# Kernel tuning notes

Measured on AMD Instinct MI355X. Metric: run time of the kernel, lower is better.

The kernel has to match this reference:

```python
import jax, jax.numpy as jnp
import numpy as np

# Module hyperparameters (from init_kwargs)
LEARNING_RATE = 0.01  # not used inside compute_weight_update
TAU_PLUS = 20.0
TAU_MINUS = 20.0
A_PLUS = 0.005
A_MINUS = 0.00525
TARGET_RATE = 0.1
HOMEOSTATIC_RATE = 0.001
TAU_HOMEOSTATIC = 1000.0

B, T, N_PRE, N_POST = 16, 8192, 128, 128


def setup_inputs() -> dict:
    key = jax.random.key(0)
    k1, k2, k3 = jax.random.split(key, 3)
    # Bernoulli spike trains at ~target_rate firing probability
    pre_spikes = (jax.random.uniform(k1, (B, T, N_PRE)) < TARGET_RATE).astype(jnp.float32)
    post_spikes = (jax.random.uniform(k2, (B, T, N_POST)) < TARGET_RATE).astype(jnp.float32)
    weights = jax.random.uniform(k3, (N_PRE, N_POST), dtype=jnp.float32)
    return {"pre_spikes": pre_spikes, "post_spikes": post_spikes, "weights": weights, "dt": 1}


def _temporal_corr(x, kernel, pad):
    """Correlate x [B,T,N] along time with 1-D kernel [L], padding pad=(lo,hi)."""
    b, t, n = x.shape
    xr = jnp.moveaxis(x, 1, 2).reshape(b * n, 1, t)  # [B*N, 1, T]
    k = kernel.reshape(1, 1, -1).astype(x.dtype)
    y = jax.lax.conv_general_dilated(
        xr, k, window_strides=(1,), padding=[pad],
        dimension_numbers=("NCH", "OIH", "NCH"))
    return jnp.moveaxis(y.reshape(b, n, t), 2, 1)  # [B,T,N]


def reference(pre_spikes, post_spikes, weights, dt):
    b, t, n_pre = pre_spikes.shape
    dt = float(dt)

    # Homeostatic rate tracking (first call: avg rates initialized to target_rate)
    alpha = dt / TAU_HOMEOSTATIC
    current_post_rate = post_spikes.mean(axis=(0, 1))
    avg_post_rate = (1.0 - alpha) * TARGET_RATE + alpha * current_post_rate

    # Truncated exponential STDP window: tau in 1..min(int(3*tau)-1, ...) = 1..59
    L = int(TAU_PLUS * 3)  # 60 taps (tau=0 tap zeroed)
    taus = jnp.arange(L, dtype=jnp.float32)
    w_plus = jnp.where(taus > 0, A_PLUS * jnp.exp(-taus * dt / TAU_PLUS), 0.0)
    w_minus = jnp.where(taus > 0, A_MINUS * jnp.exp(-taus * dt / TAU_MINUS), 0.0)

    # LTP: post_filt[t] = sum_{tau>=1} w_plus[tau] * post[t+tau] (future, zero-padded)
    post_filt = _temporal_corr(post_spikes, w_plus, (0, L - 1))
    # LTD: pre_filt[t] = sum_{tau>=1} w_minus[tau] * pre[t-tau] (past, zero-padded)
    pre_filt = _temporal_corr(pre_spikes, w_minus[::-1], (L - 1, 0))

    # sum_t mean_b outer(pre[t], post_filt[t]) - outer(pre_filt[t], post[t]), then /T
    ltp = jnp.einsum("btp,btq->pq", pre_spikes, post_filt)
    ltd = jnp.einsum("btp,btq->pq", pre_filt, post_spikes)
    stdp_update = (ltp - ltd) / (b * t)

    # Homeostatic regulation pulls post rate toward target
    post_rate_error = avg_post_rate - TARGET_RATE
    homeostatic_update = -HOMEOSTATIC_RATE * post_rate_error[None, :] * weights

    return stdp_update + homeostatic_update
```

## Files before the change

### kernel.cpp

```cpp
#include <hip/hip_runtime.h>

#define BB 16
#define TT 8192
#define NN 128
constexpr int CHUNK = 256;
constexpr int NCH   = BB * TT / CHUNK;
constexpr int NBLK  = NCH / 2;
constexpr int OUTN  = NN * NN;
constexpr int GS    = 264;
constexpr int SLOTS = OUTN / 2;
constexpr int PROWS = 315;
constexpr int NWAVE = 16;
constexpr int WIN   = CHUNK / NWAVE;

typedef _Float16 f16x8 __attribute__((ext_vector_type(8)));
typedef _Float16 f16x2 __attribute__((ext_vector_type(2)));
typedef float    f32x4 __attribute__((ext_vector_type(4)));

__device__ __forceinline__ unsigned short h16(float x) {
    _Float16 h = (_Float16)x;
    return __builtin_bit_cast(unsigned short, h);
}
__device__ __forceinline__ unsigned int pack2(float x, float y) {
    return (unsigned int)h16(x) | ((unsigned int)h16(y) << 16);
}
__device__ __forceinline__ float2 ldL(const unsigned short* p_lds, int m, int q0) {
    const unsigned int v = *(const unsigned int*)&p_lds[m * NN + q0];
    const f16x2 h = __builtin_bit_cast(f16x2, v);
    return make_float2((float)h[0], (float)h[1]);
}

template<bool ATOMIC>
__global__ __launch_bounds__(1024)
void stdp_main(const float* __restrict__ pre, const float* __restrict__ post,
               const int* __restrict__ dtp,
               unsigned int* __restrict__ part, float* __restrict__ wpost,
               float* __restrict__ outat)
{
    __shared__ __align__(16) unsigned short bufP[PROWS * NN];
    __shared__ __align__(16) unsigned short bufG[NN * GS];
    __shared__ float lds_ps[NWAVE * NN];

    const int tid    = threadIdx.x;
    const int bi     = blockIdx.x;
    const int c0g    = bi * 2;
    const int b      = c0g >> 5;
    const int chunk0 = c0g & 31;
    const int t00    = chunk0 * CHUNK;
    const int t01    = t00 + CHUNK;
    const int wv     = tid >> 6;
    const int lane   = tid & 63;

    const float dtf = (float)(*dtp);
    const float r   = expf(-dtf * (1.0f / 20.0f));

    const float* pb = post + (size_t)b * TT * NN;
    const float* ab = pre  + (size_t)b * TT * NN;

    const int sc = tid & 31;
    const int mr = tid >> 5;

    for (int m = mr; m < PROWS; m += 32) {
        const int t = t00 + 1 + m;
        const float4 v = *(const float4*)(pb + (size_t)t * NN + sc * 4);
        *(uint2*)&bufP[m * NN + sc * 4] = make_uint2(pack2(v.x, v.y), pack2(v.z, v.w));
    }
    __syncthreads();

    float4 va[10];
    #pragma unroll
    for (int i = 0; i < 10; ++i) {
        const int m = mr + i * 32;
        const int t = t01 + 1 + m;
        va[i] = make_float4(0.f, 0.f, 0.f, 0.f);
        if (m < PROWS && t < TT) va[i] = *(const float4*)(pb + (size_t)t * NN + sc * 4);
    }

    const int q0   = lane * 2;
    const int base = wv * WIN;

    unsigned int pk0[8], pk1[8];
    float ps0, ps1;
    #define FILTER_PHASE(SRC) {                                               \
        const float r2 = r * r, r3 = r2 * r, r4 = r2 * r2;                    \
        float2 p = ldL(SRC, base + 15, q0);                        \
        ps0 = p.x; ps1 = p.y;                                                 \
        float gx0 = r  * p.x, gy0 = r  * p.y;                                 \
        p = ldL(SRC, base + 16, q0);                               \
        float gx1 = r2 * p.x, gy1 = r2 * p.y;                                 \
        p = ldL(SRC, base + 17, q0);                               \
        float gx2 = r3 * p.x, gy2 = r3 * p.y;                                 \
        p = ldL(SRC, base + 18, q0);                               \
        float gx3 = r4 * p.x, gy3 = r4 * p.y;                                 \
        float wA = r * r4, wB = r2 * r4, wC = r3 * r4, wD = r4 * r4;          \
        _Pragma("unroll")                                                     \
        for (int j = 1; j < 15; ++j) {                                        \
            p = ldL(SRC, base + 15 + 4 * j, q0);                              \
            gx0 = fmaf(wA, p.x, gx0); gy0 = fmaf(wA, p.y, gy0);               \
            p = ldL(SRC, base + 16 + 4 * j, q0);                              \
            gx1 = fmaf(wB, p.x, gx1); gy1 = fmaf(wB, p.y, gy1);               \
            p = ldL(SRC, base + 17 + 4 * j, q0);                              \
            gx2 = fmaf(wC, p.x, gx2); gy2 = fmaf(wC, p.y, gy2);               \
            if (j < 14) {                                                     \
                p = ldL(SRC, base + 18 + 4 * j, q0);                          \
                gx3 = fmaf(wD, p.x, gx3); gy3 = fmaf(wD, p.y, gy3);           \
            }                                                                 \
            wA *= r4; wB *= r4; wC *= r4; wD *= r4;                           \
        }                                                                     \
        const float r8 = r4 * r4, r16 = r8 * r8, r32 = r16 * r16;             \
        const float r60 = ((r32 * r16) * r8) * r4;                            \
        float gx = (gx0 + gx1) + (gx2 + gx3);                                 \
        float gy = (gy0 + gy1) + (gy2 + gy3);                                 \
        pk0[7] = (unsigned int)h16(gx) << 16;                                 \
        pk1[7] = (unsigned int)h16(gy) << 16;                                 \
        _Pragma("unroll")                                                     \
        for (int c = 14; c >= 0; --c) {                                       \
            const float2 p1  = ldL(SRC, base + c,      q0);                   \
            const float2 p60 = ldL(SRC, base + c + 59, q0);                   \
            gx = r * (gx + p1.x) - r60 * p60.x;                               \
            gy = r * (gy + p1.y) - r60 * p60.y;                               \
            ps0 += p1.x; ps1 += p1.y;                                         \
            if (c & 1) {                                                      \
                pk0[c >> 1] = (unsigned int)h16(gx) << 16;                    \
                pk1[c >> 1] = (unsigned int)h16(gy) << 16;                    \
            } else {                                                          \
                pk0[c >> 1] |= h16(gx);                                       \
                pk1[c >> 1] |= h16(gy);                                       \
            }                                                                 \
        }                                                                     \
    }
    #define DUMP_G() {                                                        \
        unsigned short* d0 = &bufG[q0 * GS + base];                           \
        unsigned short* d1 = &bufG[(q0 + 1) * GS + base];                     \
        *(uint4*)(d0)     = make_uint4(pk0[0], pk0[1], pk0[2], pk0[3]);       \
        *(uint4*)(d0 + 8) = make_uint4(pk0[4], pk0[5], pk0[6], pk0[7]);       \
        *(uint4*)(d1)     = make_uint4(pk1[0], pk1[1], pk1[2], pk1[3]);       \
        *(uint4*)(d1 + 8) = make_uint4(pk1[4], pk1[5], pk1[6], pk1[7]);       \
        lds_ps[wv * NN + q0]     = ps0;                                       \
        lds_ps[wv * NN + q0 + 1] = ps1;                                       \
    }

    FILTER_PHASE(bufP)
    DUMP_G()
    __syncthreads();

    #pragma unroll
    for (int i = 0; i < 10; ++i) {
        const int m = mr + i * 32;
        if (m < PROWS)
            *(uint2*)&bufP[m * NN + sc * 4] =
                make_uint2(pack2(va[i].x, va[i].y), pack2(va[i].z, va[i].w));
    }

    if (tid < NN) {
        float s = 0.f;
        #pragma unroll
        for (int w = 0; w < NWAVE; ++w) s += lds_ps[w * NN + tid];
        if (chunk0 == 0) s += pb[tid];
        if constexpr (ATOMIC) atomicAdd(&wpost[tid], s);
        else wpost[(size_t)tid * NCH + c0g] = s;
    }

    const int pr0 = (wv & 7) * 16;
    const int qtb = (wv >> 3) * 4;
    f32x4 acc[4];
    #pragma unroll
    for (int qi = 0; qi < 4; ++qi) acc[qi] = (f32x4){0.f, 0.f, 0.f, 0.f};

    #define MFMA_PHASE(T0) {                                                  \
        const float* abase = ab + (size_t)((T0) + (lane >> 4) * 8) * NN + pr0 + (lane & 15); \
        float an[8];                                                          \
        _Pragma("unroll")                                                     \
        for (int j = 0; j < 8; ++j) an[j] = abase[(size_t)j * NN];            \
        _Pragma("unroll")                                                     \
        for (int ks = 0; ks < 8; ++ks) {                                      \
            f16x8 af;                                                         \
            _Pragma("unroll")                                                 \
            for (int j = 0; j < 8; ++j) af[j] = (_Float16)an[j];              \
            if (ks < 7) {                                                     \
                const float* src = abase + (size_t)((ks + 1) * 32) * NN;      \
                _Pragma("unroll")                                             \
                for (int j = 0; j < 8; ++j) an[j] = src[(size_t)j * NN];      \
            }                                                                 \
            const int koff = ks * 32 + (lane >> 4) * 8;                       \
            _Pragma("unroll")                                                 \
            for (int qi = 0; qi < 4; ++qi) {                                  \
                const f16x8 bf = *(const f16x8*)&bufG[((qtb + qi) * 16 + (lane & 15)) * GS + koff]; \
                acc[qi] = __builtin_amdgcn_mfma_f32_16x16x32_f16(af, bf, acc[qi], 0, 0, 0); \
            }                                                                 \
        }                                                                     \
    }

    MFMA_PHASE(t00)
    __syncthreads();

    FILTER_PHASE(bufP)
    DUMP_G()
    __syncthreads();

    if (tid < NN) {
        float s = 0.f;
        #pragma unroll
        for (int w = 0; w < NWAVE; ++w) s += lds_ps[w * NN + tid];
        if constexpr (ATOMIC) atomicAdd(&wpost[tid], s);
        else wpost[(size_t)tid * NCH + c0g + 1] = s;
    }

    MFMA_PHASE(t01)

    if constexpr (!ATOMIC) {
        unsigned int* dst = part + ((size_t)bi * 8 + (wv & 7)) * 1024 + lane;
        #pragma unroll
        for (int qi = 0; qi < 4; ++qi) {
            const int qt = qtb + qi;
            dst[qt * 128]      = pack2(acc[qi][0], acc[qi][1]);
            dst[qt * 128 + 64] = pack2(acc[qi][2], acc[qi][3]);
        }
    } else {
        #pragma unroll
        for (int qi = 0; qi < 4; ++qi)
            #pragma unroll
            for (int rg = 0; rg < 4; ++rg) {
                const int prow = pr0 + (lane >> 4) * 4 + rg;
                const int qcol = (qtb + qi) * 16 + (lane & 15);
                atomicAdd(&outat[prow * NN + qcol], acc[qi][rg]);
            }
    }
    #undef FILTER_PHASE
    #undef DUMP_G
    #undef MFMA_PHASE
}

__global__ __launch_bounds__(512)
void finalize_ws(const unsigned int* __restrict__ part, const float* __restrict__ wpost,
                 const int* __restrict__ dtp, const float* __restrict__ W,
                 float* __restrict__ out)
{
    __shared__ float2 red[512];
    __shared__ float  hfs[16];
    const int s    = threadIdx.x & 63;
    const int kq   = threadIdx.x >> 6;
    const int slot = blockIdx.x * 64 + s;
    const int qt   = (slot >> 7) & 7;
    const int qbase = qt * 16;

    {
        const int qi = threadIdx.x >> 5;
        const int pr = threadIdx.x & 31;
        float hsum = 0.f;
        const float* wq = wpost + (size_t)(qbase + qi) * NCH;
        #pragma unroll 4
        for (int k = pr; k < NCH; k += 32) hsum += wq[k];
        #pragma unroll
        for (int off = 16; off; off >>= 1) hsum += __shfl_down(hsum, off, 32);
        if (pr == 0) {
            const float dtf   = (float)(*dtp);
            const float alpha = dtf * 1e-3f;
            hfs[qi] = -0.001f * (alpha * (hsum * (1.0f / (float)(BB * TT)) - 0.1f));
        }
    }

    float sx = 0.f, sy = 0.f;
    #pragma unroll 8
    for (int k = kq * (NBLK / 8); k < (kq + 1) * (NBLK / 8); ++k) {
        const unsigned int v = part[(size_t)k * SLOTS + slot];
        const f16x2 h = __builtin_bit_cast(f16x2, v);
        sx += (float)h[0];
        sy += (float)h[1];
    }
    red[threadIdx.x] = make_float2(sx, sy);
    __syncthreads();
    if (threadIdx.x < 64) {
        float tx = red[s].x, ty = red[s].y;
        #pragma unroll
        for (int g = 1; g < 8; ++g) {
            const float2 v = red[g * 64 + s];
            tx += v.x; ty += v.y;
        }
        const int lane = slot & 63;
        const int rp   = (slot >> 6) & 1;
        const int wv   = slot >> 10;
        const int p    = wv * 16 + ((lane >> 4) << 2) + rp * 2;
        const int qi   = lane & 15;
        const int q    = qbase + qi;
        const float scale = (float)((0.005 - 0.00525) / (double)(BB * TT));
        const float hf = hfs[qi];
        out[p * NN + q]       = fmaf(tx, scale, hf * W[p * NN + q]);
        out[(p + 1) * NN + q] = fmaf(ty, scale, hf * W[(p + 1) * NN + q]);
    }
}

__global__ void finalize_at(const float* __restrict__ wpost, const int* __restrict__ dtp,
                            const float* __restrict__ W, float* __restrict__ out)
{
    const int i = (blockIdx.x * 256 + threadIdx.x) * 2;
    const int q = i & 127;
    const float scale = (float)((0.005 - 0.00525) / (double)(BB * TT));
    const float dtf   = (float)(*dtp);
    const float alpha = dtf * 1e-3f;
    const float inv   = 1.0f / (float)(BB * TT);
    const float hf0   = -0.001f * (alpha * (wpost[q]     * inv - 0.1f));
    const float hf1   = -0.001f * (alpha * (wpost[q + 1] * inv - 0.1f));
    float2 sv = *(const float2*)(out + i);
    float2 w  = *(const float2*)(W + i);
    float2 o;
    o.x = fmaf(sv.x, scale, hf0 * w.x);
    o.y = fmaf(sv.y, scale, hf1 * w.y);
    *(float2*)(out + i) = o;
}

extern "C" void kernel_launch(void* const* d_in, const int* in_sizes, int n_in,
                              void* d_out, int out_size, void* d_ws, size_t ws_size,
                              hipStream_t stream)
{
    const float* pre  = (const float*)d_in[0];
    const float* post = (const float*)d_in[1];
    const float* W    = (const float*)d_in[2];
    const int*   dtp  = (const int*)d_in[3];
    float* out = (float*)d_out;

    const size_t part_bytes  = (size_t)NBLK * SLOTS * sizeof(unsigned int);
    const size_t wpost_bytes = (size_t)NN * NCH * sizeof(float);
    const size_t need = part_bytes + wpost_bytes;

    if (ws_size >= need) {
        unsigned int* part = (unsigned int*)d_ws;
        float* wpost       = (float*)((char*)d_ws + part_bytes);
        hipLaunchKernelGGL((stdp_main<false>), dim3(NBLK), dim3(1024), 0, stream,
                           pre, post, dtp, part, wpost, (float*)nullptr);
        hipLaunchKernelGGL(finalize_ws, dim3(SLOTS / 64), dim3(512), 0, stream,
                           part, wpost, dtp, W, out);
    } else {
        float* wpost = (float*)d_ws;
        hipMemsetAsync(d_out, 0, OUTN * sizeof(float), stream);
        hipMemsetAsync(wpost, 0, NN * sizeof(float), stream);
        hipLaunchKernelGGL((stdp_main<true>), dim3(NBLK), dim3(1024), 0, stream,
                           pre, post, dtp, (unsigned int*)nullptr, wpost, out);
        hipLaunchKernelGGL(finalize_at, dim3(OUTN / 512), dim3(256), 0, stream,
                           wpost, dtp, W, out);
    }
}
```

Baseline: 196.2 us.

## Halve chunk size and block width, prefetch next post chunk under MFMA

Shrinks the time chunk from 256 to 128 steps and the block from 1024 to 512 threads (8 waves), doubling the number of blocks and requesting 4 blocks per CU. Each wave now covers all 8 output column tiles with 8 accumulators. The next chunk's post-spike load is issued before the first MFMA phase and written to LDS after it, so the global load can overlap compute. Per-block post-spike sums are reused via bufP instead of a separate LDS array, and the wpost layout becomes block-major. The cost is more halo reloading (60 extra rows per 128-step chunk), twice as many partial tiles for finalize to reduce, and higher register pressure from the larger accumulator set.

```diff
diff --git a/kernel.cpp b/kernel.cpp
--- a/kernel.cpp
+++ b/kernel.cpp
@@ -3,14 +3,14 @@
 #define BB 16
 #define TT 8192
 #define NN 128
-constexpr int CHUNK = 256;
-constexpr int NCH   = BB * TT / CHUNK;
-constexpr int NBLK  = NCH / 2;
+constexpr int CHUNK = 128;
+constexpr int NCHB  = BB * TT / CHUNK;
+constexpr int NBLK  = NCHB / 2;
 constexpr int OUTN  = NN * NN;
-constexpr int GS    = 264;
+constexpr int GS    = 132;
 constexpr int SLOTS = OUTN / 2;
-constexpr int PROWS = 315;
-constexpr int NWAVE = 16;
+constexpr int PROWS = 186;
+constexpr int NWAVE = 8;
 constexpr int WIN   = CHUNK / NWAVE;
 
 typedef _Float16 f16x8 __attribute__((ext_vector_type(8)));
@@ -31,7 +31,7 @@
 }
 
 template<bool ATOMIC>
-__global__ __launch_bounds__(1024)
+__global__ __launch_bounds__(512, 4)
 void stdp_main(const float* __restrict__ pre, const float* __restrict__ post,
                const int* __restrict__ dtp,
                unsigned int* __restrict__ part, float* __restrict__ wpost,
@@ -39,13 +39,12 @@
 {
     __shared__ __align__(16) unsigned short bufP[PROWS * NN];
     __shared__ __align__(16) unsigned short bufG[NN * GS];
-    __shared__ float lds_ps[NWAVE * NN];
 
     const int tid    = threadIdx.x;
     const int bi     = blockIdx.x;
     const int c0g    = bi * 2;
-    const int b      = c0g >> 5;
-    const int chunk0 = c0g & 31;
+    const int b      = c0g >> 6;
+    const int chunk0 = c0g & 63;
     const int t00    = chunk0 * CHUNK;
     const int t01    = t00 + CHUNK;
     const int wv     = tid >> 6;
@@ -60,31 +59,22 @@
     const int sc = tid & 31;
     const int mr = tid >> 5;
 
-    for (int m = mr; m < PROWS; m += 32) {
+    for (int m = mr; m < PROWS; m += 16) {
         const int t = t00 + 1 + m;
         const float4 v = *(const float4*)(pb + (size_t)t * NN + sc * 4);
         *(uint2*)&bufP[m * NN + sc * 4] = make_uint2(pack2(v.x, v.y), pack2(v.z, v.w));
     }
     __syncthreads();
 
-    float4 va[10];
-    #pragma unroll
-    for (int i = 0; i < 10; ++i) {
-        const int m = mr + i * 32;
-        const int t = t01 + 1 + m;
-        va[i] = make_float4(0.f, 0.f, 0.f, 0.f);
-        if (m < PROWS && t < TT) va[i] = *(const float4*)(pb + (size_t)t * NN + sc * 4);
-    }
-
     const int q0   = lane * 2;
     const int base = wv * WIN;
 
     unsigned int pk0[8], pk1[8];
-    float ps0, ps1;
+    float ps0 = 0.f, ps1 = 0.f;
     #define FILTER_PHASE(SRC) {                                               \
         const float r2 = r * r, r3 = r2 * r, r4 = r2 * r2;                    \
         float2 p = ldL(SRC, base + 15, q0);                        \
-        ps0 = p.x; ps1 = p.y;                                                 \
+        ps0 += p.x; ps1 += p.y;                                               \
         float gx0 = r  * p.x, gy0 = r  * p.y;                                 \
         p = ldL(SRC, base + 16, q0);                               \
         float gx1 = r2 * p.x, gy1 = r2 * p.y;                                 \
@@ -132,40 +122,33 @@
     #define DUMP_G() {                                                        \
         unsigned short* d0 = &bufG[q0 * GS + base];                           \
         unsigned short* d1 = &bufG[(q0 + 1) * GS + base];                     \
-        *(uint4*)(d0)     = make_uint4(pk0[0], pk0[1], pk0[2], pk0[3]);       \
-        *(uint4*)(d0 + 8) = make_uint4(pk0[4], pk0[5], pk0[6], pk0[7]);       \
-        *(uint4*)(d1)     = make_uint4(pk1[0], pk1[1], pk1[2], pk1[3]);       \
-        *(uint4*)(d1 + 8) = make_uint4(pk1[4], pk1[5], pk1[6], pk1[7]);       \
-        lds_ps[wv * NN + q0]     = ps0;                                       \
-        lds_ps[wv * NN + q0 + 1] = ps1;                                       \
+        *(uint4*)(d0)      = make_uint4(pk0[0], pk0[1], pk0[2], pk0[3]);      \
+        *(uint4*)(d0 + 8)  = make_uint4(pk0[4], pk0[5], pk0[6], pk0[7]);      \
+        *(uint2*)(d1)      = make_uint2(pk1[0], pk1[1]);                      \
+        *(uint2*)(d1 + 4)  = make_uint2(pk1[2], pk1[3]);                      \
+        *(uint2*)(d1 + 8)  = make_uint2(pk1[4], pk1[5]);                      \
+        *(uint2*)(d1 + 12) = make_uint2(pk1[6], pk1[7]);                      \
     }
 
     FILTER_PHASE(bufP)
     DUMP_G()
     __syncthreads();
 
+    const bool tguard = (chunk0 == 62);
+    float4 va[12];
     #pragma unroll
-    for (int i = 0; i < 10; ++i) {
-        const int m = mr + i * 32;
-        if (m < PROWS)
-            *(uint2*)&bufP[m * NN + sc * 4] =
-                make_uint2(pack2(va[i].x, va[i].y), pack2(va[i].z, va[i].w));
-    }
-
-    if (tid < NN) {
-        float s = 0.f;
-        #pragma unroll
-        for (int w = 0; w < NWAVE; ++w) s += lds_ps[w * NN + tid];
-        if (chunk0 == 0) s += pb[tid];
-        if constexpr (ATOMIC) atomicAdd(&wpost[tid], s);
-        else wpost[(size_t)tid * NCH + c0g] = s;
-    }
-
-    const int pr0 = (wv & 7) * 16;
-    const int qtb = (wv >> 3) * 4;
-    f32x4 acc[4];
+    for (int i = 0; i < 12; ++i) {
+        const int m = mr + i * 16;
+        const int t = t01 + 1 + m;
+        va[i] = make_float4(0.f, 0.f, 0.f, 0.f);
+        if (m < PROWS && (!tguard || t < TT))
+            va[i] = *(const float4*)(pb + (size_t)t * NN + sc * 4);
+    }
+
+    const int pr0 = wv * 16;
+    f32x4 acc[8];
     #pragma unroll
-    for (int qi = 0; qi < 4; ++qi) acc[qi] = (f32x4){0.f, 0.f, 0.f, 0.f};
+    for (int qt = 0; qt < 8; ++qt) acc[qt] = (f32x4){0.f, 0.f, 0.f, 0.f};
 
     #define MFMA_PHASE(T0) {                                                  \
         const float* abase = ab + (size_t)((T0) + (lane >> 4) * 8) * NN + pr0 + (lane & 15); \
@@ -173,57 +156,77 @@
         _Pragma("unroll")                                                     \
         for (int j = 0; j < 8; ++j) an[j] = abase[(size_t)j * NN];            \
         _Pragma("unroll")                                                     \
-        for (int ks = 0; ks < 8; ++ks) {                                      \
+        for (int ks = 0; ks < 4; ++ks) {                                      \
             f16x8 af;                                                         \
             _Pragma("unroll")                                                 \
             for (int j = 0; j < 8; ++j) af[j] = (_Float16)an[j];              \
-            if (ks < 7) {                                                     \
+            if (ks < 3) {                                                     \
                 const float* src = abase + (size_t)((ks + 1) * 32) * NN;      \
                 _Pragma("unroll")                                             \
                 for (int j = 0; j < 8; ++j) an[j] = src[(size_t)j * NN];      \
             }                                                                 \
             const int koff = ks * 32 + (lane >> 4) * 8;                       \
             _Pragma("unroll")                                                 \
-            for (int qi = 0; qi < 4; ++qi) {                                  \
-                const f16x8 bf = *(const f16x8*)&bufG[((qtb + qi) * 16 + (lane & 15)) * GS + koff]; \
-                acc[qi] = __builtin_amdgcn_mfma_f32_16x16x32_f16(af, bf, acc[qi], 0, 0, 0); \
+            for (int qt = 0; qt < 8; ++qt) {                                  \
+                const unsigned short* gp = &bufG[(qt * 16 + (lane & 15)) * GS + koff]; \
+                const uint2 lo = *(const uint2*)(gp);                         \
+                const uint2 hi = *(const uint2*)(gp + 4);                     \
+                const uint4 u  = make_uint4(lo.x, lo.y, hi.x, hi.y);          \
+                const f16x8 bf = __builtin_bit_cast(f16x8, u);                \
+                acc[qt] = __builtin_amdgcn_mfma_f32_16x16x32_f16(af, bf, acc[qt], 0, 0, 0); \
             }                                                                 \
         }                                                                     \
     }
 
     MFMA_PHASE(t00)
+
+    #pragma unroll
+    for (int i = 0; i < 12; ++i) {
+        const int m = mr + i * 16;
+        if (m < PROWS)
+            *(uint2*)&bufP[m * NN + sc * 4] =
+                make_uint2(pack2(va[i].x, va[i].y), pack2(va[i].z, va[i].w));
+    }
     __syncthreads();
 
     FILTER_PHASE(bufP)
     DUMP_G()
     __syncthreads();
 
+    {
+        float* psb = (float*)bufP;
+        psb[wv * NN + q0]     = ps0;
+        psb[wv * NN + q0 + 1] = ps1;
+    }
+
+    MFMA_PHASE(t01)
+    __syncthreads();
+
     if (tid < NN) {
+        const float* psb = (const float*)bufP;
         float s = 0.f;
         #pragma unroll
-        for (int w = 0; w < NWAVE; ++w) s += lds_ps[w * NN + tid];
+        for (int w = 0; w < NWAVE; ++w) s += psb[w * NN + tid];
+        if (chunk0 == 0) s += pb[tid];
         if constexpr (ATOMIC) atomicAdd(&wpost[tid], s);
-        else wpost[(size_t)tid * NCH + c0g + 1] = s;
-    }
-
-    MFMA_PHASE(t01)
+        else wpost[(size_t)bi * NN + tid] = s;
+    }
 
     if constexpr (!ATOMIC) {
-        unsigned int* dst = part + ((size_t)bi * 8 + (wv & 7)) * 1024 + lane;
-        #pragma unroll
-        for (int qi = 0; qi < 4; ++qi) {
-            const int qt = qtb + qi;
-            dst[qt * 128]      = pack2(acc[qi][0], acc[qi][1]);
-            dst[qt * 128 + 64] = pack2(acc[qi][2], acc[qi][3]);
+        unsigned int* dst = part + ((size_t)bi * 8 + wv) * 1024 + lane;
+        #pragma unroll
+        for (int qt = 0; qt < 8; ++qt) {
+            dst[qt * 128]      = pack2(acc[qt][0], acc[qt][1]);
+            dst[qt * 128 + 64] = pack2(acc[qt][2], acc[qt][3]);
         }
     } else {
         #pragma unroll
-        for (int qi = 0; qi < 4; ++qi)
+        for (int qt = 0; qt < 8; ++qt)
             #pragma unroll
             for (int rg = 0; rg < 4; ++rg) {
                 const int prow = pr0 + (lane >> 4) * 4 + rg;
-                const int qcol = (qtb + qi) * 16 + (lane & 15);
-                atomicAdd(&outat[prow * NN + qcol], acc[qi][rg]);
+                const int qcol = qt * 16 + (lane & 15);
+                atomicAdd(&outat[prow * NN + qcol], acc[qt][rg]);
             }
     }
     #undef FILTER_PHASE
@@ -248,9 +251,9 @@
         const int qi = threadIdx.x >> 5;
         const int pr = threadIdx.x & 31;
         float hsum = 0.f;
-        const float* wq = wpost + (size_t)(qbase + qi) * NCH;
+        const int q = qbase + qi;
         #pragma unroll 4
-        for (int k = pr; k < NCH; k += 32) hsum += wq[k];
+        for (int k = pr; k < NBLK; k += 32) hsum += wpost[(size_t)k * NN + q];
         #pragma unroll
         for (int off = 16; off; off >>= 1) hsum += __shfl_down(hsum, off, 32);
         if (pr == 0) {
@@ -320,13 +323,13 @@
     float* out = (float*)d_out;
 
     const size_t part_bytes  = (size_t)NBLK * SLOTS * sizeof(unsigned int);
-    const size_t wpost_bytes = (size_t)NN * NCH * sizeof(float);
+    const size_t wpost_bytes = (size_t)NBLK * NN * sizeof(float);
     const size_t need = part_bytes + wpost_bytes;
 
     if (ws_size >= need) {
         unsigned int* part = (unsigned int*)d_ws;
         float* wpost       = (float*)((char*)d_ws + part_bytes);
-        hipLaunchKernelGGL((stdp_main<false>), dim3(NBLK), dim3(1024), 0, stream,
+        hipLaunchKernelGGL((stdp_main<false>), dim3(NBLK), dim3(512), 0, stream,
                            pre, post, dtp, part, wpost, (float*)nullptr);
         hipLaunchKernelGGL(finalize_ws, dim3(SLOTS / 64), dim3(512), 0, stream,
                            part, wpost, dtp, W, out);
@@ -334,7 +337,7 @@
         float* wpost = (float*)d_ws;
         hipMemsetAsync(d_out, 0, OUTN * sizeof(float), stream);
         hipMemsetAsync(wpost, 0, NN * sizeof(float), stream);
-        hipLaunchKernelGGL((stdp_main<true>), dim3(NBLK), dim3(1024), 0, stream,
+        hipLaunchKernelGGL((stdp_main<true>), dim3(NBLK), dim3(512), 0, stream,
                            pre, post, dtp, (unsigned int*)nullptr, wpost, out);
         hipLaunchKernelGGL(finalize_at, dim3(OUTN / 512), dim3(256), 0, stream,
                            wpost, dtp, W, out);
```

After: 210.5 us. 1.07x slower.
